# Optimization experiments

Measured on AMD Instinct MI355X. Metric: run time of the kernel, lower is better.

## Reference

```python
import jax, jax.numpy as jnp
import numpy as np


def _scan_dir(x, Wih, Whh, b, reverse):
    # x: (B,T,D); Wih: (4H,D); Whh: (4H,H); b: (4H,)  (= b_ih+b_hh)
    B = x.shape[0]
    H = Whh.shape[1]
    xg = jnp.einsum('btd,gd->btg', x, Wih) + b          # (B,T,4H) precomputed input projections
    xg = jnp.swapaxes(xg, 0, 1)                          # (T,B,4H)

    def step(carry, g_t):
        h, c = carry
        g = g_t + h @ Whh.T
        i, f, gg, o = jnp.split(g, 4, axis=-1)           # PyTorch gate order: i,f,g,o
        c = jax.nn.sigmoid(f) * c + jax.nn.sigmoid(i) * jnp.tanh(gg)
        h = jax.nn.sigmoid(o) * jnp.tanh(c)
        return (h, c), h

    h0 = jnp.zeros((B, H), x.dtype)
    _, hs = jax.lax.scan(step, (h0, h0), xg, reverse=reverse)
    return jnp.swapaxes(hs, 0, 1)                        # (B,T,H), time order preserved


def _bilstm(x, Wih_f, Whh_f, b_f, Wih_b, Whh_b, b_b):
    out_f = _scan_dir(x, Wih_f, Whh_f, b_f, reverse=False)
    out_b = _scan_dir(x, Wih_b, Whh_b, b_b, reverse=True)
    return jnp.concatenate([out_f, out_b], axis=-1)      # (B,T,2H)


def setup_inputs() -> dict:
    key = jax.random.key(0)
    ks = iter(jax.random.split(key, 32))
    B, T = 1024, 128
    H1, H2 = 50, 150

    def p(shape, scale):
        return (jax.random.normal(next(ks), shape, dtype=jnp.float32) * scale)

    s1 = 1.0 / np.sqrt(H1)
    s2 = 1.0 / np.sqrt(H2)
    inp = {
        'x': jax.random.normal(next(ks), (B, 1, T), dtype=jnp.float32),
        'rrs': jax.random.normal(next(ks), (B, 4), dtype=jnp.float32),
        # layer 1: in_dim=1, H=50, bidirectional
        'l1_Wih_f': p((4 * H1, 1), s1), 'l1_Whh_f': p((4 * H1, H1), s1), 'l1_b_f': p((4 * H1,), s1),
        'l1_Wih_b': p((4 * H1, 1), s1), 'l1_Whh_b': p((4 * H1, H1), s1), 'l1_b_b': p((4 * H1,), s1),
        # layer 2: in_dim=100, H=150, bidirectional
        'l2_Wih_f': p((4 * H2, 2 * H1), s2), 'l2_Whh_f': p((4 * H2, H2), s2), 'l2_b_f': p((4 * H2,), s2),
        'l2_Wih_b': p((4 * H2, 2 * H1), s2), 'l2_Whh_b': p((4 * H2, H2), s2), 'l2_b_b': p((4 * H2,), s2),
        # heads
        'head_W': p((20, 2 * H2), 0.05), 'head_b': p((20,), 0.05),
        'pef1_W': p((10, 4), 0.05), 'pef1_b': p((10,), 0.05),
        'pef2_W': p((2, 10), 0.05), 'pef2_b': p((2,), 0.05),
        'fc_W': p((4, 30), 0.05), 'fc_b': p((4,), 0.05),
    }
    return inp


def reference(x, rrs,
              l1_Wih_f, l1_Whh_f, l1_b_f, l1_Wih_b, l1_Whh_b, l1_b_b,
              l2_Wih_f, l2_Whh_f, l2_b_f, l2_Wih_b, l2_Whh_b, l2_b_b,
              head_W, head_b, pef1_W, pef1_b, pef2_W, pef2_b, fc_W, fc_b):
    xt = jnp.transpose(x, (0, 2, 1))                     # (B,T,1)
    out1 = _bilstm(xt, l1_Wih_f, l1_Whh_f, l1_b_f, l1_Wih_b, l1_Whh_b, l1_b_b)   # (B,T,100)
    out2 = _bilstm(out1, l2_Wih_f, l2_Whh_f, l2_b_f, l2_Wih_b, l2_Whh_b, l2_b_b) # (B,T,300)
    net = out2[:, -1]                                    # (B,300)
    waveform_feat = jax.nn.leaky_relu(net @ head_W.T + head_b, 0.3)              # (B,20)
    pef = jax.nn.leaky_relu(rrs @ pef1_W.T + pef1_b, 0.3)                        # (B,10)
    pef_logits = pef @ pef2_W.T + pef2_b                                         # (B,2)
    feat = jnp.concatenate([waveform_feat, pef], axis=1)                         # (B,30)
    logits = feat @ fc_W.T + fc_b                                                # (B,4)
    return (waveform_feat, pef_logits, feat, logits)
```

## Files before the change

kernel.cpp:

```cpp
#include <hip/hip_runtime.h>


typedef unsigned short u16;
typedef unsigned int u32;
typedef float f32x4 __attribute__((ext_vector_type(4)));
typedef _Float16 f16x8 __attribute__((ext_vector_type(8)));
typedef short s16x8 __attribute__((ext_vector_type(8)));

#if __has_builtin(__builtin_amdgcn_mfma_f32_16x16x32_f16)
#define USE_F16 1
#else
#define USE_F16 0
#endif

#define B1 1024
#define TT 128

__device__ __forceinline__ u16 to_h(float x) {
#if USE_F16
    _Float16 h = (_Float16)x;
    return __builtin_bit_cast(u16, h);
#else
    u32 u = __builtin_bit_cast(u32, x);
    u32 r = u + 0x7FFFu + ((u >> 16) & 1u);
    return (u16)(r >> 16);
#endif
}
__device__ __forceinline__ float from_h(u16 s) {
#if USE_F16
    return (float)__builtin_bit_cast(_Float16, s);
#else
    u32 u = ((u32)s) << 16;
    return __builtin_bit_cast(float, u);
#endif
}

__device__ __forceinline__ f32x4 mfma16(uint4 a, uint4 b, f32x4 c) {
#if USE_F16
    return __builtin_amdgcn_mfma_f32_16x16x32_f16(
        __builtin_bit_cast(f16x8, a), __builtin_bit_cast(f16x8, b), c, 0, 0, 0);
#else
    return __builtin_amdgcn_mfma_f32_16x16x32_bf16(
        __builtin_bit_cast(s16x8, a), __builtin_bit_cast(s16x8, b), c, 0, 0, 0);
#endif
}

#define LOG2E 1.4426950408889634f
__device__ __forceinline__ float sigm(float x) {
    return __builtin_amdgcn_rcpf(1.f + __builtin_amdgcn_exp2f(-LOG2E * x));
}
__device__ __forceinline__ float tanh_(float x) {
    return 1.f - 2.f * __builtin_amdgcn_rcpf(1.f + __builtin_amdgcn_exp2f(2.f * LOG2E * x));
}
__device__ __forceinline__ float clampf(float x, float k) {
    return fminf(fmaxf(x, -k), k);
}

__device__ __forceinline__ float lstm_cell(float ig2, float fg2, float gg2,
                                           float og2, float& c)
{
    float ei = __builtin_amdgcn_exp2f(-ig2);
    float ef = __builtin_amdgcn_exp2f(-fg2);
    float eg = __builtin_amdgcn_exp2f(clampf(gg2, 43.28f));
    float P   = (1.f + ei) * (eg + 1.f);
    float num = fmaf(c, P, (eg - 1.f) * (1.f + ef));
    float cn  = num * __builtin_amdgcn_rcpf((1.f + ef) * P);
    c = cn;
    float eo = __builtin_amdgcn_exp2f(-og2);
    float ec = __builtin_amdgcn_exp2f(2.f * LOG2E * clampf(cn, 15.f));
    return (ec - 1.f) * __builtin_amdgcn_rcpf((1.f + eo) * (ec + 1.f));
}

__device__ __forceinline__ void wg_barrier_lds() {
    __builtin_amdgcn_sched_barrier(0);
    asm volatile("s_waitcnt lgkmcnt(0)" ::: "memory");
    __builtin_amdgcn_s_barrier();
    __builtin_amdgcn_sched_barrier(0);
}

__device__ __forceinline__ void prep_frag_body(
    const float* __restrict__ Wih, const float* __restrict__ Whh,
    const float* __restrict__ bias, uint4* __restrict__ dst,
    int GR, int KT, int x_off, int x_len, int h_off, int h_len, int bias_k,
    int bid, int l)
{
    int tile = bid / KT, kt = bid - tile * KT;
    int ml = l & 15;
    int qq = ml >> 2, tau = ml & 3;
    int jj = tile * 4 + qq;
    bool valid = jj < GR;
    int row = tau * GR + jj;
    float rowscale = (tau == 2) ? 2.0f * LOG2E : LOG2E;
    u32 dw[4];
    #pragma unroll
    for (int d = 0; d < 4; ++d) {
        u16 hh[2];
        #pragma unroll
        for (int s = 0; s < 2; ++s) {
            int j = d * 2 + s;
            int k = kt * 32 + (l >> 4) * 8 + j;
            float val = 0.f;
            if (valid) {
                if (k >= x_off && k < x_off + x_len) val = Wih[row * x_len + (k - x_off)];
                else if (k >= h_off && k < h_off + h_len) val = Whh[row * h_len + (k - h_off)];
                else if (k == bias_k) val = bias[row];
            }
            hh[s] = to_h(val * rowscale);
        }
        dw[d] = (u32)hh[0] | ((u32)hh[1] << 16);
    }
    uint4 o; o.x = dw[0]; o.y = dw[1]; o.z = dw[2]; o.w = dw[3];
    dst[bid * 64 + l] = o;
}

__global__ void prep_all(const float* __restrict__ W1ihF, const float* __restrict__ W1hhF,
                         const float* __restrict__ b1F,
                         const float* __restrict__ W1ihB, const float* __restrict__ W1hhB,
                         const float* __restrict__ b1B,
                         const float* __restrict__ W2ihF, const float* __restrict__ W2hhF,
                         const float* __restrict__ b2F, const float* __restrict__ W2ihB,
                         uint4* __restrict__ frag1f, uint4* __restrict__ frag1b,
                         uint4* __restrict__ frag2f, float* __restrict__ WtT)
{
    int bid = blockIdx.x;
    int l = threadIdx.x;
    if (bid < 32)
        prep_frag_body(W1ihF, W1hhF, b1F, frag1f, 50, 2, 0, 1, 1, 50, 63, bid, l);
    else if (bid < 64)
        prep_frag_body(W1ihB, W1hhB, b1B, frag1b, 50, 2, 0, 1, 1, 50, 63, bid - 32, l);
    else if (bid < 384)
        prep_frag_body(W2ihF, W2hhF, b2F, frag2f, 150, 8, 0, 100, 100, 150, 255, bid - 64, l);
    else {
        int idx = (bid - 384) * 64 + l;
        if (idx < 60000) {
            int k = idx / 600, g = idx - k * 600;
            WtT[idx] = W2ihB[g * 100 + k];
        }
    }
}

__global__ __launch_bounds__(512, 2) void l1_scan(
    const float* __restrict__ x, const uint4* __restrict__ fragF,
    const uint4* __restrict__ fragB, u16* __restrict__ out1f)
{
    const int tid = threadIdx.x;
    const int lane = tid & 63;
    const int w = tid >> 6;
    const int q = lane >> 4;
    const int b = lane & 15;
    const int blk = blockIdx.x;
    const int dir = blockIdx.y;
    const uint4* frag = dir ? fragB : fragF;

    __shared__ u16 v[2][1024];
    __shared__ float x_s[128][17];

    uint4 af[2][2];
    #pragma unroll
    for (int p = 0; p < 2; ++p)
        #pragma unroll
        for (int kt = 0; kt < 2; ++kt)
            af[p][kt] = frag[((w + 8 * p) * 2 + kt) * 64 + lane];

    const int b0 = blk * 16;
    for (int idx = tid; idx < 1024; idx += 512) ((u32*)v)[idx] = 0u;
    for (int idx = tid; idx < 2048; idx += 512) {
        int bb = idx >> 7, t = idx & 127;
        x_s[t][bb] = x[(size_t)(b0 + bb) * TT + t];
    }
    __syncthreads();
    const u16 oneh = to_h(1.0f);
    if (tid < 16) {
        v[0][(112 + tid) * 8 + 7] = oneh;
        v[1][(112 + tid) * 8 + 7] = oneh;
        v[0][tid * 8] = to_h(x[(size_t)(b0 + tid) * TT + (dir ? TT - 1 : 0)]);
    }
    int vslot[2]; size_t eb[2];
    #pragma unroll
    for (int p = 0; p < 2; ++p) {
        int jj = (w + 8 * p) * 4 + q;
        int k1 = 1 + (jj < 50 ? jj : 0);
        vslot[p] = ((k1 >> 5) * 64 + ((k1 & 31) >> 3) * 16 + b) * 8 + (k1 & 7);
        int k2 = dir * 50 + (jj < 50 ? jj : 0);
        eb[p] = (((size_t)blk * 4 + (k2 >> 5)) * 64
                 + ((k2 & 31) >> 3) * 16 + b) * 8 + (k2 & 7);
    }
    float c[2] = {0.f, 0.f};
    __syncthreads();

#define L1_STEP(T, CUR) { \
    uint4 bf0 = *(const uint4*)&v[CUR][lane * 8]; \
    uint4 bf1 = *(const uint4*)&v[CUR][(64 + lane) * 8]; \
    f32x4 acc[2]; \
    _Pragma("unroll") for (int p = 0; p < 2; ++p) { \
        acc[p] = mfma16(af[p][0], bf0, (f32x4){0.f, 0.f, 0.f, 0.f}); \
        acc[p] = mfma16(af[p][1], bf1, acc[p]); \
    } \
    const int tt = dir ? 127 - (T) : (T); \
    _Pragma("unroll") for (int p = 0; p < 2; ++p) { \
        int jj = (w + 8 * p) * 4 + q; \
        if (jj < 50) { \
            float hn = lstm_cell(acc[p][0], acc[p][1], acc[p][2], acc[p][3], c[p]); \
            u16 hb = to_h(hn); \
            out1f[eb[p] + (size_t)tt * 131072] = hb; \
            v[1 - (CUR)][vslot[p]] = hb; \
        } \
    } \
    if (tid < 16 && (T) < 127) \
        v[1 - (CUR)][tid * 8] = to_h(x_s[dir ? 126 - (T) : (T) + 1][tid]); \
    wg_barrier_lds(); }

    for (int t2 = 0; t2 < TT; t2 += 2) {
        L1_STEP(t2, 0)
        L1_STEP(t2 + 1, 1)
    }
#undef L1_STEP
}

__global__ __launch_bounds__(512, 2) void l2f_scan(
    const uint4* __restrict__ frag, const u16* __restrict__ out1f,
    float* __restrict__ net)
{
    const int tid = threadIdx.x;
    const int lane = tid & 63;
    const int w = tid >> 6;
    const int q = lane >> 4;
    const int b = lane & 15;
    const int blk = blockIdx.x;
    const int b0 = blk * 16;
    const uint4* o4 = (const uint4*)out1f;

    __shared__ u16 v[2][4096];

    uint4 af[5][8];
    #pragma unroll
    for (int i = 0; i < 5; ++i)
        #pragma unroll
        for (int kt = 0; kt < 8; ++kt)
            af[i][kt] = frag[((w + 8 * i) * 8 + kt) * 64 + lane];

    for (int idx = tid; idx < 4096; idx += 512) ((u32*)v)[idx] = 0u;

    const uint4* pfp = o4 + (size_t)blk * 256 + lane;
    uint4 pfA[4], pfB[4];
    #pragma unroll
    for (int ktx = 0; ktx < 4; ++ktx) pfA[ktx] = pfp[ktx * 64];
    pfp += 16384;
    #pragma unroll
    for (int ktx = 0; ktx < 4; ++ktx) pfB[ktx] = pfp[ktx * 64];
    pfp += 16384;

    __syncthreads();
    const u16 oneh = to_h(1.0f);
    if (tid < 16) {
        v[0][(496 + tid) * 8 + 7] = oneh;
        v[1][(496 + tid) * 8 + 7] = oneh;
    }
    if (w == 0 && lane < 16) {
        uint2 xv; xv.x = pfA[3].x; xv.y = pfA[3].y;
        *(uint2*)&v[0][(192 + lane) * 8] = xv;
    }

    int vslot[5];
    #pragma unroll
    for (int p = 0; p < 5; ++p) {
        int jj = (w + 8 * p) * 4 + q;
        int k = 100 + (jj < 150 ? jj : 0);
        vslot[p] = ((k >> 5) * 64 + ((k & 31) >> 3) * 16 + b) * 8 + (k & 7);
    }
    float c[5] = {0.f, 0.f, 0.f, 0.f, 0.f};

    f32x4 accA[5], accB[5];
    #pragma unroll
    for (int p = 0; p < 5; ++p) {
        accA[p] = mfma16(af[p][0], pfA[0], (f32x4){0.f, 0.f, 0.f, 0.f});
        accA[p] = mfma16(af[p][1], pfA[1], accA[p]);
        accA[p] = mfma16(af[p][2], pfA[2], accA[p]);
    }
    __syncthreads();

#define L2F_STEP(T, CUR, ACCC, ACCN, PFREF, PFOTH) { \
    uint4 bfu[5]; \
    _Pragma("unroll") for (int kh = 0; kh < 5; ++kh) \
        bfu[kh] = *(const uint4*)&v[CUR][((kh + 3) * 64 + lane) * 8]; \
    _Pragma("unroll") for (int kh = 0; kh < 5; ++kh) { \
        _Pragma("unroll") for (int p = 0; p < 5; ++p) \
            ACCC[p] = mfma16(af[p][kh + 3], bfu[kh], ACCC[p]); \
    } \
    _Pragma("unroll") for (int ktx = 0; ktx < 4; ++ktx) \
        PFREF[ktx] = pfp[ktx * 64]; \
    pfp += 16384; \
    _Pragma("unroll") for (int p = 0; p < 5; ++p) { \
        ACCN[p] = mfma16(af[p][0], PFOTH[0], (f32x4){0.f, 0.f, 0.f, 0.f}); \
        ACCN[p] = mfma16(af[p][1], PFOTH[1], ACCN[p]); \
        ACCN[p] = mfma16(af[p][2], PFOTH[2], ACCN[p]); \
        int jj = (w + 8 * p) * 4 + q; \
        if (jj < 150) { \
            float hn = lstm_cell(ACCC[p][0], ACCC[p][1], ACCC[p][2], ACCC[p][3], c[p]); \
            v[1 - (CUR)][vslot[p]] = to_h(hn); \
            if ((T) == 127) net[(size_t)(b0 + b) * 300 + jj] = hn; \
        } \
    } \
    if (w == 0 && lane < 16) { \
        uint2 xv; xv.x = PFOTH[3].x; xv.y = PFOTH[3].y; \
        *(uint2*)&v[1 - (CUR)][(192 + lane) * 8] = xv; \
    } \
    wg_barrier_lds(); }

    for (int t2 = 0; t2 < TT; t2 += 2) {
        L2F_STEP(t2, 0, accA, accB, pfA, pfB)
        L2F_STEP(t2 + 1, 1, accB, accA, pfB, pfA)
    }
#undef L2F_STEP
}

__global__ __launch_bounds__(640, 1) void l2b_step(
    const u16* __restrict__ out1f, const float* __restrict__ WtT,
    const float* __restrict__ bias, float* __restrict__ net)
{
    const int tid = threadIdx.x;
    const int blk = blockIdx.x;
    const int b0 = blk * 16;
    __shared__ alignas(16) float x_s[100][16];
    __shared__ alignas(16) float gbuf[16][644];
    for (int idx = tid; idx < 1600; idx += 640) {
        int k2 = idx >> 4, bb = idx & 15;
        x_s[k2][bb] = from_h(out1f[((((size_t)127 * 64 + blk) * 4 + (k2 >> 5)) * 64
                                    + ((k2 & 31) >> 3) * 16 + bb) * 8 + (k2 & 7)]);
    }
    __syncthreads();
    if (tid < 600) {
        int g = tid;
        float acc[16];
        #pragma unroll
        for (int bb = 0; bb < 16; ++bb) acc[bb] = 0.f;
        for (int k = 0; k < 100; ++k) {
            float wv = WtT[k * 600 + g];
            float4 xa = *(const float4*)&x_s[k][0];
            float4 xb = *(const float4*)&x_s[k][4];
            float4 xc = *(const float4*)&x_s[k][8];
            float4 xd = *(const float4*)&x_s[k][12];
            acc[0] = fmaf(wv, xa.x, acc[0]);  acc[1] = fmaf(wv, xa.y, acc[1]);
            acc[2] = fmaf(wv, xa.z, acc[2]);  acc[3] = fmaf(wv, xa.w, acc[3]);
            acc[4] = fmaf(wv, xb.x, acc[4]);  acc[5] = fmaf(wv, xb.y, acc[5]);
            acc[6] = fmaf(wv, xb.z, acc[6]);  acc[7] = fmaf(wv, xb.w, acc[7]);
            acc[8] = fmaf(wv, xc.x, acc[8]);  acc[9] = fmaf(wv, xc.y, acc[9]);
            acc[10] = fmaf(wv, xc.z, acc[10]); acc[11] = fmaf(wv, xc.w, acc[11]);
            acc[12] = fmaf(wv, xd.x, acc[12]); acc[13] = fmaf(wv, xd.y, acc[13]);
            acc[14] = fmaf(wv, xd.z, acc[14]); acc[15] = fmaf(wv, xd.w, acc[15]);
        }
        #pragma unroll
        for (int bb = 0; bb < 16; ++bb) gbuf[bb][g] = acc[bb];
    }
    __syncthreads();
    for (int idx = tid; idx < 2400; idx += 640) {
        int j = idx >> 4, bb = idx & 15;
        float ig = gbuf[bb][j]       + bias[j];
        float gg = gbuf[bb][j + 300] + bias[j + 300];
        float og = gbuf[bb][j + 450] + bias[j + 450];
        float cn = sigm(ig) * tanh_(gg);
        float hn = sigm(og) * tanh_(cn);
        net[(size_t)(b0 + bb) * 300 + 150 + j] = hn;
    }
}

__global__ void head1(const float* __restrict__ net, const float* __restrict__ rrs,
                      const float* __restrict__ headW, const float* __restrict__ headb,
                      const float* __restrict__ p1W, const float* __restrict__ p1b,
                      const float* __restrict__ p2W, const float* __restrict__ p2b,
                      float* __restrict__ out)
{
    int gid = blockIdx.x * 256 + threadIdx.x;
    int b = gid >> 2, og = gid & 3;
    float acc[5];
    #pragma unroll
    for (int o2 = 0; o2 < 5; ++o2) acc[o2] = headb[og * 5 + o2];
    const float* nb = net + (size_t)b * 300;
    for (int k = 0; k < 300; ++k) {
        float nv = nb[k];
        #pragma unroll
        for (int o2 = 0; o2 < 5; ++o2)
            acc[o2] = fmaf(headW[(og * 5 + o2) * 300 + k], nv, acc[o2]);
    }
    #pragma unroll
    for (int o2 = 0; o2 < 5; ++o2) {
        int o = og * 5 + o2;
        float vv = acc[o2] > 0.f ? acc[o2] : 0.3f * acc[o2];
        out[b * 20 + o] = vv;
        out[22528 + b * 30 + o] = vv;
    }
    if (og == 0) {
        float p[10];
        #pragma unroll
        for (int r = 0; r < 10; ++r) {
            float a = p1b[r];
            #pragma unroll
            for (int qq = 0; qq < 4; ++qq) a = fmaf(p1W[r * 4 + qq], rrs[b * 4 + qq], a);
            p[r] = a > 0.f ? a : 0.3f * a;
            out[22528 + b * 30 + 20 + r] = p[r];
        }
        #pragma unroll
        for (int s = 0; s < 2; ++s) {
            float a = p2b[s];
            #pragma unroll
            for (int r = 0; r < 10; ++r) a = fmaf(p2W[s * 10 + r], p[r], a);
            out[20480 + b * 2 + s] = a;
        }
    }
}

__global__ void head2(const float* __restrict__ fcW, const float* __restrict__ fcb,
                      float* __restrict__ out)
{
    int b = blockIdx.x * 256 + threadIdx.x;
    const float* feat = out + 22528 + b * 30;
    float f[30];
    #pragma unroll
    for (int k = 0; k < 30; ++k) f[k] = feat[k];
    #pragma unroll
    for (int s = 0; s < 4; ++s) {
        float a = fcb[s];
        #pragma unroll
        for (int k = 0; k < 30; ++k) a = fmaf(fcW[s * 30 + k], f[k], a);
        out[53248 + b * 4 + s] = a;
    }
}

extern "C" void kernel_launch(void* const* d_in, const int* in_sizes, int n_in,
                              void* d_out, int out_size, void* d_ws, size_t ws_size,
                              hipStream_t stream)
{
    const float* x     = (const float*)d_in[0];
    const float* rrs   = (const float*)d_in[1];
    const float* W1ihF = (const float*)d_in[2];
    const float* W1hhF = (const float*)d_in[3];
    const float* b1F   = (const float*)d_in[4];
    const float* W1ihB = (const float*)d_in[5];
    const float* W1hhB = (const float*)d_in[6];
    const float* b1B   = (const float*)d_in[7];
    const float* W2ihF = (const float*)d_in[8];
    const float* W2hhF = (const float*)d_in[9];
    const float* b2F   = (const float*)d_in[10];
    const float* W2ihB = (const float*)d_in[11];
    const float* b2B   = (const float*)d_in[13];
    const float* headW = (const float*)d_in[14];
    const float* headb = (const float*)d_in[15];
    const float* p1W   = (const float*)d_in[16];
    const float* p1b   = (const float*)d_in[17];
    const float* p2W   = (const float*)d_in[18];
    const float* p2b   = (const float*)d_in[19];
    const float* fcW   = (const float*)d_in[20];
    const float* fcb   = (const float*)d_in[21];
    float* out = (float*)d_out;

    char* ws = (char*)d_ws;
    uint4* frag1f = (uint4*)(ws + 0);
    uint4* frag1b = (uint4*)(ws + 32768);
    uint4* frag2f = (uint4*)(ws + 65536);
    float* WtT    = (float*)(ws + 393216);
    u16*   out1f  = (u16*)(ws + 655360);
    float* net    = (float*)(ws + 655360 + 33554432);
    (void)ws_size; (void)in_sizes; (void)n_in; (void)out_size;

    prep_all<<<1322, 64, 0, stream>>>(W1ihF, W1hhF, b1F, W1ihB, W1hhB, b1B,
                                      W2ihF, W2hhF, b2F, W2ihB,
                                      frag1f, frag1b, frag2f, WtT);
    l1_scan<<<dim3(64, 2), 512, 0, stream>>>(x, frag1f, frag1b, out1f);
    l2f_scan<<<64, 512, 0, stream>>>(frag2f, out1f, net);
    l2b_step<<<64, 640, 0, stream>>>(out1f, WtT, b2B, net);
    head1<<<16, 256, 0, stream>>>(net, rrs, headW, headb, p1W, p1b, p2W, p2b, out);
    head2<<<4, 256, 0, stream>>>(fcW, fcb, out);
}
```

Before: 274.5 us.

## Stagger MFMA and cell phases across warp halves in layer-2 forward recurrence

Splits the layer-2 forward step into phases (loads, input-projection MFMAs, recurrent MFMAs, LSTM cell math). Warps 0-3 run the next step's input MFMAs before the recurrent MFMAs, while warps 4+ run them after the cell update. Scheduling barriers pin this order. The intent is to spread matrix-core work and transcendental/VALU work across warps within each barrier interval so they overlap, at the cost of divergent code paths and possibly longer critical paths for some warps.

```diff
diff --git a/kernel.cpp b/kernel.cpp
--- a/kernel.cpp
+++ b/kernel.cpp
@@ -279,39 +279,76 @@
     }
     __syncthreads();
 
-#define L2F_STEP(T, CUR, ACCC, ACCN, PFREF, PFOTH) { \
+#define L2F_PRE(CUR, PFREF) \
     uint4 bfu[5]; \
     _Pragma("unroll") for (int kh = 0; kh < 5; ++kh) \
         bfu[kh] = *(const uint4*)&v[CUR][((kh + 3) * 64 + lane) * 8]; \
+    _Pragma("unroll") for (int ktx = 0; ktx < 4; ++ktx) \
+        PFREF[ktx] = pfp[ktx * 64]; \
+    pfp += 16384;
+
+#define L2F_HMFMA(ACCC) \
     _Pragma("unroll") for (int kh = 0; kh < 5; ++kh) { \
         _Pragma("unroll") for (int p = 0; p < 5; ++p) \
             ACCC[p] = mfma16(af[p][kh + 3], bfu[kh], ACCC[p]); \
-    } \
-    _Pragma("unroll") for (int ktx = 0; ktx < 4; ++ktx) \
-        PFREF[ktx] = pfp[ktx * 64]; \
-    pfp += 16384; \
+    }
+
+#define L2F_XMFMA(ACCN, PFOTH) \
     _Pragma("unroll") for (int p = 0; p < 5; ++p) { \
         ACCN[p] = mfma16(af[p][0], PFOTH[0], (f32x4){0.f, 0.f, 0.f, 0.f}); \
         ACCN[p] = mfma16(af[p][1], PFOTH[1], ACCN[p]); \
         ACCN[p] = mfma16(af[p][2], PFOTH[2], ACCN[p]); \
+    }
+
+#define L2F_CELLS(T, CUR, ACCC) \
+    _Pragma("unroll") for (int p = 0; p < 5; ++p) { \
         int jj = (w + 8 * p) * 4 + q; \
         if (jj < 150) { \
             float hn = lstm_cell(ACCC[p][0], ACCC[p][1], ACCC[p][2], ACCC[p][3], c[p]); \
             v[1 - (CUR)][vslot[p]] = to_h(hn); \
             if ((T) == 127) net[(size_t)(b0 + b) * 300 + jj] = hn; \
         } \
-    } \
+    }
+
+#define L2F_STEP_A(T, CUR, ACCC, ACCN, PFREF, PFOTH) { \
+    L2F_PRE(CUR, PFREF) \
+    L2F_XMFMA(ACCN, PFOTH) \
     if (w == 0 && lane < 16) { \
         uint2 xv; xv.x = PFOTH[3].x; xv.y = PFOTH[3].y; \
         *(uint2*)&v[1 - (CUR)][(192 + lane) * 8] = xv; \
     } \
+    __builtin_amdgcn_sched_barrier(0); \
+    L2F_HMFMA(ACCC) \
+    __builtin_amdgcn_sched_barrier(0); \
+    L2F_CELLS(T, CUR, ACCC) \
     wg_barrier_lds(); }
 
-    for (int t2 = 0; t2 < TT; t2 += 2) {
-        L2F_STEP(t2, 0, accA, accB, pfA, pfB)
-        L2F_STEP(t2 + 1, 1, accB, accA, pfB, pfA)
-    }
-#undef L2F_STEP
+#define L2F_STEP_B(T, CUR, ACCC, ACCN, PFREF, PFOTH) { \
+    L2F_PRE(CUR, PFREF) \
+    L2F_HMFMA(ACCC) \
+    __builtin_amdgcn_sched_barrier(0); \
+    L2F_CELLS(T, CUR, ACCC) \
+    __builtin_amdgcn_sched_barrier(0); \
+    L2F_XMFMA(ACCN, PFOTH) \
+    wg_barrier_lds(); }
+
+    if (w < 4) {
+        for (int t2 = 0; t2 < TT; t2 += 2) {
+            L2F_STEP_A(t2, 0, accA, accB, pfA, pfB)
+            L2F_STEP_A(t2 + 1, 1, accB, accA, pfB, pfA)
+        }
+    } else {
+        for (int t2 = 0; t2 < TT; t2 += 2) {
+            L2F_STEP_B(t2, 0, accA, accB, pfA, pfB)
+            L2F_STEP_B(t2 + 1, 1, accB, accA, pfB, pfA)
+        }
+    }
+#undef L2F_STEP_A
+#undef L2F_STEP_B
+#undef L2F_PRE
+#undef L2F_HMFMA
+#undef L2F_XMFMA
+#undef L2F_CELLS
 }
 
 __global__ __launch_bounds__(640, 1) void l2b_step(
```

New measurement: 292.7 us. +6.6%, slower.

## Merge forward and backward layer-1 scans into one 1024-thread workgroup

Applied to the files above, without the earlier changes.

The layer-1 scan launch changes from a 64x2 grid of 512-thread blocks (one direction per block) to 64 blocks of 1024 threads. Waves 0-7 run the forward direction and waves 8-15 the backward direction, each with its own double-buffered LDS state vector. The x tile is loaded into shared memory once per batch tile, where each direction's block used to load it separately. The cost is that the per-step workgroup barrier now synchronizes both directions together, and halving the block count may reduce how many CUs are busy.

```diff
diff --git a/kernel.cpp b/kernel.cpp
--- a/kernel.cpp
+++ b/kernel.cpp
@@ -139,20 +139,21 @@
     }
 }
 
-__global__ __launch_bounds__(512, 2) void l1_scan(
+__global__ __launch_bounds__(1024, 2) void l1_scan(
     const float* __restrict__ x, const uint4* __restrict__ fragF,
     const uint4* __restrict__ fragB, u16* __restrict__ out1f)
 {
     const int tid = threadIdx.x;
     const int lane = tid & 63;
     const int w = tid >> 6;
+    const int dir = w >> 3;
+    const int wl = w & 7;
     const int q = lane >> 4;
     const int b = lane & 15;
     const int blk = blockIdx.x;
-    const int dir = blockIdx.y;
     const uint4* frag = dir ? fragB : fragF;
 
-    __shared__ u16 v[2][1024];
+    __shared__ u16 v[2][2][1024];
     __shared__ float x_s[128][17];
 
     uint4 af[2][2];
@@ -160,25 +161,28 @@
     for (int p = 0; p < 2; ++p)
         #pragma unroll
         for (int kt = 0; kt < 2; ++kt)
-            af[p][kt] = frag[((w + 8 * p) * 2 + kt) * 64 + lane];
+            af[p][kt] = frag[((wl + 8 * p) * 2 + kt) * 64 + lane];
 
     const int b0 = blk * 16;
-    for (int idx = tid; idx < 1024; idx += 512) ((u32*)v)[idx] = 0u;
-    for (int idx = tid; idx < 2048; idx += 512) {
+    for (int idx = tid; idx < 2048; idx += 1024) ((u32*)v)[idx] = 0u;
+    for (int idx = tid; idx < 2048; idx += 1024) {
         int bb = idx >> 7, t = idx & 127;
         x_s[t][bb] = x[(size_t)(b0 + bb) * TT + t];
     }
     __syncthreads();
     const u16 oneh = to_h(1.0f);
     if (tid < 16) {
-        v[0][(112 + tid) * 8 + 7] = oneh;
-        v[1][(112 + tid) * 8 + 7] = oneh;
-        v[0][tid * 8] = to_h(x[(size_t)(b0 + tid) * TT + (dir ? TT - 1 : 0)]);
+        v[0][0][(112 + tid) * 8 + 7] = oneh;
+        v[0][1][(112 + tid) * 8 + 7] = oneh;
+        v[1][0][(112 + tid) * 8 + 7] = oneh;
+        v[1][1][(112 + tid) * 8 + 7] = oneh;
+        v[0][0][tid * 8] = to_h(x[(size_t)(b0 + tid) * TT + 0]);
+        v[1][0][tid * 8] = to_h(x[(size_t)(b0 + tid) * TT + (TT - 1)]);
     }
     int vslot[2]; size_t eb[2];
     #pragma unroll
     for (int p = 0; p < 2; ++p) {
-        int jj = (w + 8 * p) * 4 + q;
+        int jj = (wl + 8 * p) * 4 + q;
         int k1 = 1 + (jj < 50 ? jj : 0);
         vslot[p] = ((k1 >> 5) * 64 + ((k1 & 31) >> 3) * 16 + b) * 8 + (k1 & 7);
         int k2 = dir * 50 + (jj < 50 ? jj : 0);
@@ -189,8 +193,8 @@
     __syncthreads();
 
 #define L1_STEP(T, CUR) { \
-    uint4 bf0 = *(const uint4*)&v[CUR][lane * 8]; \
-    uint4 bf1 = *(const uint4*)&v[CUR][(64 + lane) * 8]; \
+    uint4 bf0 = *(const uint4*)&v[dir][CUR][lane * 8]; \
+    uint4 bf1 = *(const uint4*)&v[dir][CUR][(64 + lane) * 8]; \
     f32x4 acc[2]; \
     _Pragma("unroll") for (int p = 0; p < 2; ++p) { \
         acc[p] = mfma16(af[p][0], bf0, (f32x4){0.f, 0.f, 0.f, 0.f}); \
@@ -198,16 +202,16 @@
     } \
     const int tt = dir ? 127 - (T) : (T); \
     _Pragma("unroll") for (int p = 0; p < 2; ++p) { \
-        int jj = (w + 8 * p) * 4 + q; \
+        int jj = (wl + 8 * p) * 4 + q; \
         if (jj < 50) { \
             float hn = lstm_cell(acc[p][0], acc[p][1], acc[p][2], acc[p][3], c[p]); \
             u16 hb = to_h(hn); \
             out1f[eb[p] + (size_t)tt * 131072] = hb; \
-            v[1 - (CUR)][vslot[p]] = hb; \
+            v[dir][1 - (CUR)][vslot[p]] = hb; \
         } \
     } \
-    if (tid < 16 && (T) < 127) \
-        v[1 - (CUR)][tid * 8] = to_h(x_s[dir ? 126 - (T) : (T) + 1][tid]); \
+    if (lane < 16 && wl == 0 && (T) < 127) \
+        v[dir][1 - (CUR)][lane * 8] = to_h(x_s[dir ? 126 - (T) : (T) + 1][lane]); \
     wg_barrier_lds(); }
 
     for (int t2 = 0; t2 < TT; t2 += 2) {
@@ -465,7 +469,7 @@
     prep_all<<<1322, 64, 0, stream>>>(W1ihF, W1hhF, b1F, W1ihB, W1hhB, b1B,
                                       W2ihF, W2hhF, b2F, W2ihB,
                                       frag1f, frag1b, frag2f, WtT);
-    l1_scan<<<dim3(64, 2), 512, 0, stream>>>(x, frag1f, frag1b, out1f);
+    l1_scan<<<64, 1024, 0, stream>>>(x, frag1f, frag1b, out1f);
     l2f_scan<<<64, 512, 0, stream>>>(frag2f, out1f, net);
     l2b_step<<<64, 640, 0, stream>>>(out1f, WtT, b2B, net);
     head1<<<16, 256, 0, stream>>>(net, rrs, headW, headb, p1W, p1b, p2W, p2b, out);
```

New measurement: 308.3 us. 12.3% more time.
